# Performance work log

Measured on AMD Instinct MI355X. Metric: run time of the kernel, lower is better.

The kernel has to match this reference:

```python
import jax, jax.numpy as jnp
import numpy as np

STATE_DIM = 512
ACTION_FEAT_DIM = 64
HIDDEN = 256


def setup_inputs() -> dict:
    key = jax.random.key(0)
    ks = jax.random.split(key, 8)
    B, K = 256, 1000
    state_embed = jax.random.normal(ks[0], (B, STATE_DIM), dtype=jnp.float32)
    action_feats = jax.random.normal(ks[1], (B, K, ACTION_FEAT_DIM), dtype=jnp.float32)
    s = 0.05
    W1 = jax.random.normal(ks[2], (STATE_DIM + ACTION_FEAT_DIM, HIDDEN), dtype=jnp.float32) * s
    b1 = jnp.zeros((HIDDEN,), dtype=jnp.float32)
    W2 = jax.random.normal(ks[3], (HIDDEN, HIDDEN // 2), dtype=jnp.float32) * s
    b2 = jnp.zeros((HIDDEN // 2,), dtype=jnp.float32)
    W3 = jax.random.normal(ks[4], (HIDDEN // 2, 1), dtype=jnp.float32) * s
    b3 = jnp.zeros((1,), dtype=jnp.float32)
    return {"state_embed": state_embed, "action_feats": action_feats,
            "W1": W1, "b1": b1, "W2": W2, "b2": b2, "W3": W3, "b3": b3}


def reference(state_embed, action_feats, W1, b1, W2, b2, W3, b3):
    # Faithful math: concat([state broadcast to K, action_feats]) -> Linear/ReLU x2 -> Linear(1)
    # Efficient form: split W1 rows so state part is computed once per batch row.
    W1_s = W1[:STATE_DIM]            # [state_dim, hidden]
    W1_a = W1[STATE_DIM:]            # [action_feat_dim, hidden]
    h_state = state_embed @ W1_s     # [B, hidden]
    h = jax.nn.relu(jnp.einsum('bkf,fh->bkh', action_feats, W1_a) + h_state[:, None, :] + b1)
    h = jax.nn.relu(jnp.einsum('bkh,hg->bkg', h, W2) + b2)
    logits = (jnp.einsum('bkg,go->bko', h, W3) + b3)[..., 0]  # [B, K]
    return logits
```

## Files before the change

kernel.cpp:

```cpp
#include <hip/hip_runtime.h>

typedef _Float16 f16;
typedef f16 f16x4 __attribute__((ext_vector_type(4)));
typedef f16 f16x8 __attribute__((ext_vector_type(8)));
typedef float f32x4 __attribute__((ext_vector_type(4)));


#define AF_STRIDE 72
#define H1_STRIDE 264

__global__ __launch_bounds__(256) void prep_kernel(const float* __restrict__ W1,
                                                   const float* __restrict__ W2,
                                                   const float* __restrict__ state,
                                                   const float* __restrict__ b1,
                                                   f16* __restrict__ pw1at,
                                                   f16* __restrict__ pw2,
                                                   float* __restrict__ hstate) {
    __shared__ float srow[4][512];
    int blk = blockIdx.x;
    int tid = threadIdx.x;
    if (blk < 24) {
        int idx = blk * 256 + tid;
        int F = idx >> 6;
        int L = idx & 63;
        int q = L >> 4, c = L & 15;
        f16x8 v;
        if (F < 32) {
            int mt = F >> 1, kt = F & 1;
            #pragma unroll
            for (int j = 0; j < 8; ++j) {
                int f = kt * 32 + q * 8 + j;
                v[j] = (f16)W1[(size_t)(512 + f) * 256 + mt * 16 + c];
            }
            *(f16x8*)(pw1at + ((size_t)F * 64 + L) * 8) = v;
        } else {
            int F2 = F - 32;
            int nt = F2 >> 3, kt = F2 & 7;
            #pragma unroll
            for (int j = 0; j < 8; ++j) {
                int k = kt * 32 + q * 8 + j;
                v[j] = (f16)W2[(size_t)k * 128 + nt * 16 + c];
            }
            *(f16x8*)(pw2 + ((size_t)F2 * 64 + L) * 8) = v;
        }
    } else {
        int b0 = (blk - 24) * 4;
        #pragma unroll
        for (int i = 0; i < 8; ++i) {
            int e = i * 256 + tid;
            srow[e >> 9][e & 511] = state[(size_t)b0 * 512 + e];
        }
        __syncthreads();
        float bias = b1[tid];
        float a0 = bias, a1 = bias, a2 = bias, a3 = bias;
        for (int f = 0; f < 512; ++f) {
            float wv = W1[(size_t)f * 256 + tid];
            a0 = fmaf(srow[0][f], wv, a0);
            a1 = fmaf(srow[1][f], wv, a1);
            a2 = fmaf(srow[2][f], wv, a2);
            a3 = fmaf(srow[3][f], wv, a3);
        }
        hstate[(size_t)(b0 + 0) * 256 + tid] = a0;
        hstate[(size_t)(b0 + 1) * 256 + tid] = a1;
        hstate[(size_t)(b0 + 2) * 256 + tid] = a2;
        hstate[(size_t)(b0 + 3) * 256 + tid] = a3;
    }
}

__global__ __launch_bounds__(256) void fused_kernel(const float* __restrict__ afeat,
                                                    const float* __restrict__ hstate,
                                                    const f16* __restrict__ pw1at,
                                                    const f16* __restrict__ pw2,
                                                    const float* __restrict__ b2,
                                                    const float* __restrict__ W3,
                                                    const float* __restrict__ b3,
                                                    float* __restrict__ out) {
    __shared__ f16 afs[64 * AF_STRIDE];
    __shared__ f16 h1s[64 * H1_STRIDE];
    __shared__ float lds3[256];

    int tid = threadIdx.x;
    int w = tid >> 6;
    int L = tid & 63;
    int q = L >> 4, c = L & 15;
    int r0 = blockIdx.x * 64;

    f16x8 a1f[4][2];
    #pragma unroll
    for (int i = 0; i < 4; ++i)
        #pragma unroll
        for (int kt = 0; kt < 2; ++kt)
            a1f[i][kt] = *(const f16x8*)(pw1at + ((size_t)((4 * w + i) * 2 + kt) * 64 + L) * 8);

    #pragma unroll
    for (int i = 0; i < 4; ++i) {
        int e = i * 256 + tid;
        int row = e >> 4, c4 = e & 15;
        f32x4 v = *(const f32x4*)(afeat + (size_t)(r0 + row) * 64 + c4 * 4);
        f16x4 hv;
        hv[0] = (f16)v[0]; hv[1] = (f16)v[1]; hv[2] = (f16)v[2]; hv[3] = (f16)v[3];
        *(f16x4*)(afs + row * AF_STRIDE + c4 * 4) = hv;
    }
    __syncthreads();

    f16x8 bf[4][2];
    #pragma unroll
    for (int nt = 0; nt < 4; ++nt)
        #pragma unroll
        for (int kt = 0; kt < 2; ++kt)
            bf[nt][kt] = *(const f16x8*)(afs + (nt * 16 + c) * AF_STRIDE + kt * 32 + q * 8);

    f32x4 acc1[4][4];
    #pragma unroll
    for (int i = 0; i < 4; ++i)
        #pragma unroll
        for (int nt = 0; nt < 4; ++nt)
            acc1[i][nt] = (f32x4){0.f, 0.f, 0.f, 0.f};

    #pragma unroll
    for (int i = 0; i < 4; ++i)
        #pragma unroll
        for (int nt = 0; nt < 4; ++nt)
            #pragma unroll
            for (int kt = 0; kt < 2; ++kt)
                acc1[i][nt] = __builtin_amdgcn_mfma_f32_16x16x32_f16(
                    a1f[i][kt], bf[nt][kt], acc1[i][nt], 0, 0, 0);

    int b0i = r0 / 1000;
    int boundary = (b0i + 1) * 1000;
    int b1i = b0i < 255 ? b0i + 1 : 255;
    #pragma unroll
    for (int i = 0; i < 4; ++i) {
        int hbase = (4 * w + i) * 16 + q * 4;
        f32x4 hsA = *(const f32x4*)(hstate + (size_t)b0i * 256 + hbase);
        f32x4 hsB = *(const f32x4*)(hstate + (size_t)b1i * 256 + hbase);
        #pragma unroll
        for (int nt = 0; nt < 4; ++nt) {
            int rowg = r0 + nt * 16 + c;
            bool sel = rowg >= boundary;
            f16x4 hv;
            #pragma unroll
            for (int reg = 0; reg < 4; ++reg) {
                float v = acc1[i][nt][reg] + (sel ? hsB[reg] : hsA[reg]);
                v = v > 0.f ? v : 0.f;
                hv[reg] = (f16)v;
            }
            *(f16x4*)(h1s + (nt * 16 + c) * H1_STRIDE + hbase) = hv;
        }
    }
    __syncthreads();

    f32x4 acc2[4][2];
    #pragma unroll
    for (int rb = 0; rb < 4; ++rb) {
        acc2[rb][0] = (f32x4){0.f, 0.f, 0.f, 0.f};
        acc2[rb][1] = (f32x4){0.f, 0.f, 0.f, 0.f};
    }
    #pragma unroll
    for (int kt = 0; kt < 8; ++kt) {
        f16x8 a2[4];
        #pragma unroll
        for (int rb = 0; rb < 4; ++rb)
            a2[rb] = *(const f16x8*)(h1s + (rb * 16 + c) * H1_STRIDE + kt * 32 + q * 8);
        #pragma unroll
        for (int ntl = 0; ntl < 2; ++ntl) {
            f16x8 bfr = *(const f16x8*)(pw2 + ((size_t)((w * 2 + ntl) * 8 + kt) * 64 + L) * 8);
            #pragma unroll
            for (int rb = 0; rb < 4; ++rb)
                acc2[rb][ntl] = __builtin_amdgcn_mfma_f32_16x16x32_f16(
                    a2[rb], bfr, acc2[rb][ntl], 0, 0, 0);
        }
    }

    float b2v[2], w3v[2];
    #pragma unroll
    for (int ntl = 0; ntl < 2; ++ntl) {
        int col = (w * 2 + ntl) * 16 + c;
        b2v[ntl] = b2[col];
        w3v[ntl] = W3[col];
    }
    #pragma unroll
    for (int rb = 0; rb < 4; ++rb) {
        #pragma unroll
        for (int reg = 0; reg < 4; ++reg) {
            float p = 0.f;
            #pragma unroll
            for (int ntl = 0; ntl < 2; ++ntl) {
                float v = acc2[rb][ntl][reg] + b2v[ntl];
                v = v > 0.f ? v : 0.f;
                p = fmaf(v, w3v[ntl], p);
            }
            p += __shfl_xor(p, 1);
            p += __shfl_xor(p, 2);
            p += __shfl_xor(p, 4);
            p += __shfl_xor(p, 8);
            if (c == 0) lds3[(rb * 16 + q * 4 + reg) * 4 + w] = p;
        }
    }
    __syncthreads();
    if (tid < 64) {
        f32x4 s = *(const f32x4*)(lds3 + tid * 4);
        out[r0 + tid] = s[0] + s[1] + s[2] + s[3] + b3[0];
    }
}

extern "C" void kernel_launch(void* const* d_in, const int* in_sizes, int n_in,
                              void* d_out, int out_size, void* d_ws, size_t ws_size,
                              hipStream_t stream) {
    const float* state = (const float*)d_in[0];
    const float* afeat = (const float*)d_in[1];
    const float* W1    = (const float*)d_in[2];
    const float* b1    = (const float*)d_in[3];
    const float* W2    = (const float*)d_in[4];
    const float* b2    = (const float*)d_in[5];
    const float* W3    = (const float*)d_in[6];
    const float* b3    = (const float*)d_in[7];
    float* out = (float*)d_out;

    float* hstate = (float*)d_ws;
    f16* pw1at = (f16*)((char*)d_ws + 65536 * sizeof(float));
    f16* pw2   = pw1at + 16384;

    prep_kernel<<<88, 256, 0, stream>>>(W1, W2, state, b1, pw1at, pw2, hstate);
    fused_kernel<<<4000, 256, 0, stream>>>(afeat, hstate, pw1at, pw2, b2, W3, b3, out);
}
```

Baseline: 156.0 us.

## Process four row tiles per block with register-resident W2 and transposed shuffle reduction

The fused kernel now handles 256 rows per block in a loop over four 64-row tiles. It stages all action features up front and keeps the W2 fragments in registers for the whole block, so the per-tile W2 global loads and per-block setup are amortised. The final reduction uses a transpose-style butterfly that cuts shuffle count, and the prep kernel spreads the state projection over one block per batch row. Launch bounds of (256,2) and a larger LDS footprint may limit occupancy and reduce how much load latency the GPU can hide, and the extra syncs per tile serialise work inside a block.

```diff
diff --git a/kernel.cpp b/kernel.cpp
--- a/kernel.cpp
+++ b/kernel.cpp
@@ -16,7 +16,7 @@
                                                    f16* __restrict__ pw1at,
                                                    f16* __restrict__ pw2,
                                                    float* __restrict__ hstate) {
-    __shared__ float srow[4][512];
+    __shared__ float srow[512];
     int blk = blockIdx.x;
     int tid = threadIdx.x;
     if (blk < 24) {
@@ -44,46 +44,37 @@
             *(f16x8*)(pw2 + ((size_t)F2 * 64 + L) * 8) = v;
         }
     } else {
-        int b0 = (blk - 24) * 4;
-        #pragma unroll
-        for (int i = 0; i < 8; ++i) {
-            int e = i * 256 + tid;
-            srow[e >> 9][e & 511] = state[(size_t)b0 * 512 + e];
-        }
+        int b = blk - 24;
+        srow[tid] = state[(size_t)b * 512 + tid];
+        srow[tid + 256] = state[(size_t)b * 512 + 256 + tid];
         __syncthreads();
-        float bias = b1[tid];
-        float a0 = bias, a1 = bias, a2 = bias, a3 = bias;
-        for (int f = 0; f < 512; ++f) {
-            float wv = W1[(size_t)f * 256 + tid];
-            a0 = fmaf(srow[0][f], wv, a0);
-            a1 = fmaf(srow[1][f], wv, a1);
-            a2 = fmaf(srow[2][f], wv, a2);
-            a3 = fmaf(srow[3][f], wv, a3);
-        }
-        hstate[(size_t)(b0 + 0) * 256 + tid] = a0;
-        hstate[(size_t)(b0 + 1) * 256 + tid] = a1;
-        hstate[(size_t)(b0 + 2) * 256 + tid] = a2;
-        hstate[(size_t)(b0 + 3) * 256 + tid] = a3;
+        float a0 = 0.f, a1 = 0.f;
+        #pragma unroll 8
+        for (int f = 0; f < 512; f += 2) {
+            a0 = fmaf(srow[f],     W1[(size_t)f * 256 + tid],       a0);
+            a1 = fmaf(srow[f + 1], W1[(size_t)(f + 1) * 256 + tid], a1);
+        }
+        hstate[(size_t)b * 256 + tid] = a0 + a1 + b1[tid];
     }
 }
 
-__global__ __launch_bounds__(256) void fused_kernel(const float* __restrict__ afeat,
-                                                    const float* __restrict__ hstate,
-                                                    const f16* __restrict__ pw1at,
-                                                    const f16* __restrict__ pw2,
-                                                    const float* __restrict__ b2,
-                                                    const float* __restrict__ W3,
-                                                    const float* __restrict__ b3,
-                                                    float* __restrict__ out) {
-    __shared__ f16 afs[64 * AF_STRIDE];
+__global__ __launch_bounds__(256, 2) void fused_kernel(const float* __restrict__ afeat,
+                                                       const float* __restrict__ hstate,
+                                                       const f16* __restrict__ pw1at,
+                                                       const f16* __restrict__ pw2,
+                                                       const float* __restrict__ b2,
+                                                       const float* __restrict__ W3,
+                                                       const float* __restrict__ b3,
+                                                       float* __restrict__ out) {
+    __shared__ f16 afs4[256 * AF_STRIDE];
     __shared__ f16 h1s[64 * H1_STRIDE];
-    __shared__ float lds3[256];
+    __shared__ float lds3[64 * 6];
 
     int tid = threadIdx.x;
     int w = tid >> 6;
     int L = tid & 63;
     int q = L >> 4, c = L & 15;
-    int r0 = blockIdx.x * 64;
+    int r0g = blockIdx.x * 256;
 
     f16x8 a1f[4][2];
     #pragma unroll
@@ -91,87 +82,27 @@
         #pragma unroll
         for (int kt = 0; kt < 2; ++kt)
             a1f[i][kt] = *(const f16x8*)(pw1at + ((size_t)((4 * w + i) * 2 + kt) * 64 + L) * 8);
-
-    #pragma unroll
-    for (int i = 0; i < 4; ++i) {
-        int e = i * 256 + tid;
-        int row = e >> 4, c4 = e & 15;
-        f32x4 v = *(const f32x4*)(afeat + (size_t)(r0 + row) * 64 + c4 * 4);
-        f16x4 hv;
-        hv[0] = (f16)v[0]; hv[1] = (f16)v[1]; hv[2] = (f16)v[2]; hv[3] = (f16)v[3];
-        *(f16x4*)(afs + row * AF_STRIDE + c4 * 4) = hv;
-    }
-    __syncthreads();
-
-    f16x8 bf[4][2];
-    #pragma unroll
-    for (int nt = 0; nt < 4; ++nt)
-        #pragma unroll
-        for (int kt = 0; kt < 2; ++kt)
-            bf[nt][kt] = *(const f16x8*)(afs + (nt * 16 + c) * AF_STRIDE + kt * 32 + q * 8);
-
-    f32x4 acc1[4][4];
-    #pragma unroll
-    for (int i = 0; i < 4; ++i)
-        #pragma unroll
-        for (int nt = 0; nt < 4; ++nt)
-            acc1[i][nt] = (f32x4){0.f, 0.f, 0.f, 0.f};
-
-    #pragma unroll
-    for (int i = 0; i < 4; ++i)
-        #pragma unroll
-        for (int nt = 0; nt < 4; ++nt)
-            #pragma unroll
-            for (int kt = 0; kt < 2; ++kt)
-                acc1[i][nt] = __builtin_amdgcn_mfma_f32_16x16x32_f16(
-                    a1f[i][kt], bf[nt][kt], acc1[i][nt], 0, 0, 0);
-
-    int b0i = r0 / 1000;
-    int boundary = (b0i + 1) * 1000;
-    int b1i = b0i < 255 ? b0i + 1 : 255;
-    #pragma unroll
-    for (int i = 0; i < 4; ++i) {
-        int hbase = (4 * w + i) * 16 + q * 4;
-        f32x4 hsA = *(const f32x4*)(hstate + (size_t)b0i * 256 + hbase);
-        f32x4 hsB = *(const f32x4*)(hstate + (size_t)b1i * 256 + hbase);
-        #pragma unroll
-        for (int nt = 0; nt < 4; ++nt) {
-            int rowg = r0 + nt * 16 + c;
-            bool sel = rowg >= boundary;
-            f16x4 hv;
-            #pragma unroll
-            for (int reg = 0; reg < 4; ++reg) {
-                float v = acc1[i][nt][reg] + (sel ? hsB[reg] : hsA[reg]);
-                v = v > 0.f ? v : 0.f;
-                hv[reg] = (f16)v;
-            }
-            *(f16x4*)(h1s + (nt * 16 + c) * H1_STRIDE + hbase) = hv;
-        }
-    }
-    __syncthreads();
-
-    f32x4 acc2[4][2];
-    #pragma unroll
-    for (int rb = 0; rb < 4; ++rb) {
-        acc2[rb][0] = (f32x4){0.f, 0.f, 0.f, 0.f};
-        acc2[rb][1] = (f32x4){0.f, 0.f, 0.f, 0.f};
-    }
-    #pragma unroll
-    for (int kt = 0; kt < 8; ++kt) {
-        f16x8 a2[4];
-        #pragma unroll
-        for (int rb = 0; rb < 4; ++rb)
-            a2[rb] = *(const f16x8*)(h1s + (rb * 16 + c) * H1_STRIDE + kt * 32 + q * 8);
-        #pragma unroll
-        for (int ntl = 0; ntl < 2; ++ntl) {
-            f16x8 bfr = *(const f16x8*)(pw2 + ((size_t)((w * 2 + ntl) * 8 + kt) * 64 + L) * 8);
-            #pragma unroll
-            for (int rb = 0; rb < 4; ++rb)
-                acc2[rb][ntl] = __builtin_amdgcn_mfma_f32_16x16x32_f16(
-                    a2[rb], bfr, acc2[rb][ntl], 0, 0, 0);
-        }
-    }
-
+    f16x8 w2b[2][8];
+    #pragma unroll
+    for (int ntl = 0; ntl < 2; ++ntl)
+        #pragma unroll
+        for (int kt = 0; kt < 8; ++kt)
+            w2b[ntl][kt] = *(const f16x8*)(pw2 + ((size_t)((w * 2 + ntl) * 8 + kt) * 64 + L) * 8);
+
+    #pragma unroll
+    for (int i = 0; i < 8; ++i) {
+        int id = i * 256 + tid;
+        int row = id >> 3, c32 = id & 7;
+        const float* p = afeat + (size_t)(r0g + row) * 64 + c32 * 8;
+        f32x4 lo = *(const f32x4*)p;
+        f32x4 hi = *(const f32x4*)(p + 4);
+        f16x8 v;
+        v[0] = (f16)lo[0]; v[1] = (f16)lo[1]; v[2] = (f16)lo[2]; v[3] = (f16)lo[3];
+        v[4] = (f16)hi[0]; v[5] = (f16)hi[1]; v[6] = (f16)hi[2]; v[7] = (f16)hi[3];
+        *(f16x8*)(afs4 + row * AF_STRIDE + c32 * 8) = v;
+    }
+
+    float b3v = b3[0];
     float b2v[2], w3v[2];
     #pragma unroll
     for (int ntl = 0; ntl < 2; ++ntl) {
@@ -179,28 +110,117 @@
         b2v[ntl] = b2[col];
         w3v[ntl] = W3[col];
     }
-    #pragma unroll
-    for (int rb = 0; rb < 4; ++rb) {
-        #pragma unroll
-        for (int reg = 0; reg < 4; ++reg) {
-            float p = 0.f;
-            #pragma unroll
-            for (int ntl = 0; ntl < 2; ++ntl) {
-                float v = acc2[rb][ntl][reg] + b2v[ntl];
-                v = v > 0.f ? v : 0.f;
-                p = fmaf(v, w3v[ntl], p);
-            }
-            p += __shfl_xor(p, 1);
-            p += __shfl_xor(p, 2);
-            p += __shfl_xor(p, 4);
-            p += __shfl_xor(p, 8);
-            if (c == 0) lds3[(rb * 16 + q * 4 + reg) * 4 + w] = p;
-        }
-    }
     __syncthreads();
-    if (tid < 64) {
-        f32x4 s = *(const f32x4*)(lds3 + tid * 4);
-        out[r0 + tid] = s[0] + s[1] + s[2] + s[3] + b3[0];
+
+    for (int t = 0; t < 4; ++t) {
+        int r0 = r0g + t * 64;
+
+        f16x8 bf[4][2];
+        #pragma unroll
+        for (int nt = 0; nt < 4; ++nt)
+            #pragma unroll
+            for (int kt = 0; kt < 2; ++kt)
+                bf[nt][kt] = *(const f16x8*)(afs4 + (t * 64 + nt * 16 + c) * AF_STRIDE + kt * 32 + q * 8);
+
+        f32x4 acc1[4][4];
+        #pragma unroll
+        for (int i = 0; i < 4; ++i)
+            #pragma unroll
+            for (int nt = 0; nt < 4; ++nt)
+                acc1[i][nt] = (f32x4){0.f, 0.f, 0.f, 0.f};
+        #pragma unroll
+        for (int i = 0; i < 4; ++i)
+            #pragma unroll
+            for (int nt = 0; nt < 4; ++nt)
+                #pragma unroll
+                for (int kt = 0; kt < 2; ++kt)
+                    acc1[i][nt] = __builtin_amdgcn_mfma_f32_16x16x32_f16(
+                        a1f[i][kt], bf[nt][kt], acc1[i][nt], 0, 0, 0);
+
+        int b0i = r0 / 1000;
+        int boundary = (b0i + 1) * 1000;
+        int b1i = b0i < 255 ? b0i + 1 : 255;
+        #pragma unroll
+        for (int i = 0; i < 4; ++i) {
+            int hbase = (4 * w + i) * 16 + q * 4;
+            f32x4 hsA = *(const f32x4*)(hstate + (size_t)b0i * 256 + hbase);
+            f32x4 hsB = *(const f32x4*)(hstate + (size_t)b1i * 256 + hbase);
+            #pragma unroll
+            for (int nt = 0; nt < 4; ++nt) {
+                bool sel = (r0 + nt * 16 + c) >= boundary;
+                f16x4 hv;
+                #pragma unroll
+                for (int reg = 0; reg < 4; ++reg) {
+                    float v = acc1[i][nt][reg] + (sel ? hsB[reg] : hsA[reg]);
+                    v = v > 0.f ? v : 0.f;
+                    hv[reg] = (f16)v;
+                }
+                *(f16x4*)(h1s + (nt * 16 + c) * H1_STRIDE + hbase) = hv;
+            }
+        }
+        __syncthreads();
+
+        f32x4 acc2[4][2];
+        #pragma unroll
+        for (int rb = 0; rb < 4; ++rb) {
+            acc2[rb][0] = (f32x4){0.f, 0.f, 0.f, 0.f};
+            acc2[rb][1] = (f32x4){0.f, 0.f, 0.f, 0.f};
+        }
+        #pragma unroll
+        for (int kt = 0; kt < 8; ++kt) {
+            f16x8 a2[4];
+            #pragma unroll
+            for (int rb = 0; rb < 4; ++rb)
+                a2[rb] = *(const f16x8*)(h1s + (rb * 16 + c) * H1_STRIDE + kt * 32 + q * 8);
+            #pragma unroll
+            for (int ntl = 0; ntl < 2; ++ntl)
+                #pragma unroll
+                for (int rb = 0; rb < 4; ++rb)
+                    acc2[rb][ntl] = __builtin_amdgcn_mfma_f32_16x16x32_f16(
+                        a2[rb], w2b[ntl][kt], acc2[rb][ntl], 0, 0, 0);
+        }
+
+        float p[16];
+        #pragma unroll
+        for (int rb = 0; rb < 4; ++rb)
+            #pragma unroll
+            for (int reg = 0; reg < 4; ++reg) {
+                float v0 = acc2[rb][0][reg] + b2v[0]; v0 = v0 > 0.f ? v0 : 0.f;
+                float v1 = acc2[rb][1][reg] + b2v[1]; v1 = v1 > 0.f ? v1 : 0.f;
+                p[rb * 4 + reg] = fmaf(v0, w3v[0], v1 * w3v[1]);
+            }
+        float s0[8];
+        #pragma unroll
+        for (int i = 0; i < 8; ++i) {
+            float send = (c & 1) ? p[2 * i] : p[2 * i + 1];
+            float keep = (c & 1) ? p[2 * i + 1] : p[2 * i];
+            s0[i] = keep + __shfl_xor(send, 1);
+        }
+        float s1[4];
+        #pragma unroll
+        for (int i = 0; i < 4; ++i) {
+            float send = (c & 2) ? s0[2 * i] : s0[2 * i + 1];
+            float keep = (c & 2) ? s0[2 * i + 1] : s0[2 * i];
+            s1[i] = keep + __shfl_xor(send, 2);
+        }
+        float s2[2];
+        #pragma unroll
+        for (int i = 0; i < 2; ++i) {
+            float send = (c & 4) ? s1[2 * i] : s1[2 * i + 1];
+            float keep = (c & 4) ? s1[2 * i + 1] : s1[2 * i];
+            s2[i] = keep + __shfl_xor(send, 4);
+        }
+        float send3 = (c & 8) ? s2[0] : s2[1];
+        float keep3 = (c & 8) ? s2[1] : s2[0];
+        float s3 = keep3 + __shfl_xor(send3, 8);
+        int m = (c >> 2) * 16 + q * 4 + (c & 3);
+        lds3[m * 6 + w] = s3;
+        __syncthreads();
+
+        if (tid < 64) {
+            const float* pm = lds3 + tid * 6;
+            out[r0 + tid] = pm[0] + pm[1] + pm[2] + pm[3] + b3v;
+        }
     }
 }
 
@@ -221,6 +241,6 @@
     f16* pw1at = (f16*)((char*)d_ws + 65536 * sizeof(float));
     f16* pw2   = pw1at + 16384;
 
-    prep_kernel<<<88, 256, 0, stream>>>(W1, W2, state, b1, pw1at, pw2, hstate);
-    fused_kernel<<<4000, 256, 0, stream>>>(afeat, hstate, pw1at, pw2, b2, W3, b3, out);
+    prep_kernel<<<280, 256, 0, stream>>>(W1, W2, state, b1, pw1at, pw2, hstate);
+    fused_kernel<<<1000, 256, 0, stream>>>(afeat, hstate, pw1at, pw2, b2, W3, b3, out);
 }
```

After: 140.1 us. 10.2% less time.
